# Performance work log

Hardware: AMD Instinct MI355X
Metric: run time of the kernel (lower is better)

The kernel has to match this reference:

```python
import jax, jax.numpy as jnp
import numpy as np

B, N, M, D, CD, H, DH = 2, 2048, 2048, 1024, 1024, 8, 64
INNER = H * DH  # 512
FFD = 4 * D
SCALE = DH ** -0.5


def _ln(x, g, b):
    mu = jnp.mean(x, axis=-1, keepdims=True)
    var = jnp.mean((x - mu) ** 2, axis=-1, keepdims=True)
    return (x - mu) * jax.lax.rsqrt(var + 1e-5) * g + b


def _ff(x, g, b, w1, b1, w2, b2):
    h = jax.nn.gelu(_ln(x, g, b) @ w1 + b1, approximate=False)
    return h @ w2 + b2


def setup_inputs() -> dict:
    key = jax.random.key(0)
    ks = jax.random.split(key, 16)
    s = 0.02
    return {
        'x': jax.random.normal(ks[0], (B, N, D), jnp.float32),
        'context': jax.random.normal(ks[1], (B, M, CD), jnp.float32),
        'mask': jnp.ones((B, N), bool),
        'context_mask': jnp.ones((B, M), bool),
        'ln_x_g': jnp.ones(D), 'ln_x_b': jnp.zeros(D),
        'ln_c_g': jnp.ones(CD), 'ln_c_b': jnp.zeros(CD),
        'W_qk': jax.random.normal(ks[2], (D, INNER)) * s,
        'W_v': jax.random.normal(ks[3], (D, INNER)) * s,
        'Wc_qk': jax.random.normal(ks[4], (CD, INNER)) * s,
        'Wc_v': jax.random.normal(ks[5], (CD, INNER)) * s,
        'W_out': jax.random.normal(ks[6], (INNER, D)) * s, 'b_out': jnp.zeros(D),
        'Wc_out': jax.random.normal(ks[7], (INNER, CD)) * s, 'bc_out': jnp.zeros(CD),
        'ff_g': jnp.ones(D), 'ff_b': jnp.zeros(D),
        'ff_w1': jax.random.normal(ks[8], (D, FFD)) * s, 'ff_b1': jnp.zeros(FFD),
        'ff_w2': jax.random.normal(ks[9], (FFD, D)) * s, 'ff_b2': jnp.zeros(D),
        'cff_g': jnp.ones(CD), 'cff_b': jnp.zeros(CD),
        'cff_w1': jax.random.normal(ks[10], (CD, FFD)) * s, 'cff_b1': jnp.zeros(FFD),
        'cff_w2': jax.random.normal(ks[11], (FFD, CD)) * s, 'cff_b2': jnp.zeros(CD),
    }


def reference(x, context, mask, context_mask,
              ln_x_g, ln_x_b, ln_c_g, ln_c_b,
              W_qk, W_v, Wc_qk, Wc_v, W_out, b_out, Wc_out, bc_out,
              ff_g, ff_b, ff_w1, ff_b1, ff_w2, ff_b2,
              cff_g, cff_b, cff_w1, cff_b1, cff_w2, cff_b2):
    # pre-norm bidirectional cross attention
    xn = _ln(x, ln_x_g, ln_x_b)
    cn = _ln(context, ln_c_g, ln_c_b)
    qk = (xn @ W_qk).reshape(B, N, H, DH)      # b i h d
    v = (xn @ W_v).reshape(B, N, H, DH)
    cqk = (cn @ Wc_qk).reshape(B, M, H, DH)    # b j h d
    cv = (cn @ Wc_v).reshape(B, M, H, DH)
    sim = jnp.einsum('bihd,bjhd->bhij', qk, cqk) * SCALE
    pair_mask = mask[:, None, :, None] & context_mask[:, None, None, :]
    big_neg = jnp.finfo(sim.dtype).max
    sim = jnp.where(pair_mask, sim, -big_neg)
    attn = jax.nn.softmax(sim, axis=-1)        # x attends over context (j)
    cattn = jax.nn.softmax(sim, axis=-2)       # context attends over x (i)
    out = jnp.einsum('bhij,bjhd->bihd', attn, cv).reshape(B, N, INNER)
    cout = jnp.einsum('bhij,bihd->bjhd', cattn, v).reshape(B, M, INNER)
    x = x + (out @ W_out + b_out)
    context = context + (cout @ Wc_out + bc_out)
    # dual pre-norm FFN residual
    x = _ff(x, ff_g, ff_b, ff_w1, ff_b1, ff_w2, ff_b2) + x
    context = _ff(context, cff_g, cff_b, cff_w1, cff_b1, cff_w2, cff_b2) + context
    return (x, context)
```

## Files before the change

### kernel.cpp

```cpp
#include <hip/hip_runtime.h>
#include <hip/hip_bf16.h>
#include <cmath>

typedef __hip_bfloat16 bf16;
typedef __attribute__((ext_vector_type(8))) short short8;
typedef __attribute__((ext_vector_type(4))) short short4g;
typedef __attribute__((ext_vector_type(4))) float f32x4;

#define B_     2
#define N_     2048
#define M_     2048
#define D_     1024
#define H_     8
#define DH_    64
#define INNER_ 512
#define FFD_   4096
#define ROWS   4096

__device__ __forceinline__ float b2f(bf16 x){ return __bfloat162float(x); }
__device__ __forceinline__ bf16  f2b(float x){ return __float2bfloat16(x); }
__device__ __forceinline__ float s2f(short s){
    unsigned u = ((unsigned)(unsigned short)s) << 16;
    float f; __builtin_memcpy(&f, &u, 4); return f;
}
__device__ __forceinline__ short f2s(float f){
    bf16 b = __float2bfloat16(f);
    short s; __builtin_memcpy(&s, &b, 2); return s;
}
__device__ __forceinline__ float ldx(const void* p, size_t i, bool isb){
    return isb ? __bfloat162float(((const bf16*)p)[i]) : ((const float*)p)[i];
}
__device__ __forceinline__ void stx(void* p, size_t i, float v, bool isb){
    if (isb) ((bf16*)p)[i] = f2b(v); else ((float*)p)[i] = v;
}
__device__ __forceinline__ void gld16(const bf16* g, bf16* l){
    __builtin_amdgcn_global_load_lds(
        (const __attribute__((address_space(1))) void*)g,
        (__attribute__((address_space(3))) void*)l, 16, 0, 0);
}
__device__ __forceinline__ short8 ds_read128(const bf16* p){
    unsigned a = (unsigned)(size_t)(const __attribute__((address_space(3))) bf16*)p;
    short8 r;
    asm volatile("ds_read_b128 %0, %1" : "=v"(r) : "v"(a));
    return r;
}

__global__ void probe_kernel(const void* ones, int* flag){
    unsigned w = *(const unsigned*)ones;
    *flag = (w == 0x3F803F80u) ? 1 : 0;
}

template<bool IN_EXT>
__global__ __launch_bounds__(256) void ln_kernel(const void* __restrict__ x,
    const void* __restrict__ g, const void* __restrict__ b,
    bf16* __restrict__ out, const int* __restrict__ flagp)
{
    const int C = 1024;
    bool f = (*flagp != 0);
    bool bx = IN_EXT ? f : true;
    size_t base = (size_t)blockIdx.x * C;
    int t = threadIdx.x;
    float v[4]; float s = 0.f;
#pragma unroll
    for (int q = 0; q < 4; q++){ v[q] = ldx(x, base + t + q*256, bx); s += v[q]; }
    __shared__ float red[256];
    red[t] = s; __syncthreads();
    for (int o = 128; o > 0; o >>= 1){ if (t < o) red[t] += red[t+o]; __syncthreads(); }
    float mu = red[0] * (1.0f/1024.0f);
    __syncthreads();
    s = 0.f;
#pragma unroll
    for (int q = 0; q < 4; q++){ float d = v[q]-mu; s += d*d; }
    red[t] = s; __syncthreads();
    for (int o = 128; o > 0; o >>= 1){ if (t < o) red[t] += red[t+o]; __syncthreads(); }
    float rstd = rsqrtf(red[0]*(1.0f/1024.0f) + 1e-5f);
    bf16* orow = out + base;
#pragma unroll
    for (int q = 0; q < 4; q++){
        int i = t + q*256;
        orow[i] = f2b((v[q]-mu)*rstd*ldx(g,i,f) + ldx(b,i,f));
    }
}

__global__ __launch_bounds__(256) void tcast_kernel(
    const void* __restrict__ in, bf16* __restrict__ out,
    int R, int Ccols, size_t ibs, size_t obs, int force_b16,
    const int* __restrict__ flagp)
{
    bool isb = force_b16 ? true : (*flagp != 0);
    __shared__ float T[32][33];
    size_t ib = (size_t)blockIdx.z * ibs, ob = (size_t)blockIdx.z * obs;
    int r0 = blockIdx.x * 32, c0 = blockIdx.y * 32;
    int tx = threadIdx.x & 31, ty = threadIdx.x >> 5;
#pragma unroll
    for (int rr = 0; rr < 32; rr += 8)
        T[ty + rr][tx] = ldx(in, ib + (size_t)(r0 + ty + rr) * Ccols + c0 + tx, isb);
    __syncthreads();
#pragma unroll
    for (int rr = 0; rr < 32; rr += 8)
        out[ob + (size_t)(c0 + ty + rr) * R + r0 + tx] = f2b(T[tx][ty + rr]);
}

template<int MODE, int EPI, int DP>
__global__ __launch_bounds__(256) void mfma_gemm(
    const bf16* __restrict__ A, const bf16* __restrict__ A2,
    const bf16* __restrict__ Bt,
    const void* __restrict__ bias, const void* __restrict__ bias2,
    const void* __restrict__ res,  const void* __restrict__ res2,
    void* __restrict__ C, void* __restrict__ C2,
    int K, int lda, int ldb, int ldc,
    size_t coff, size_t cstr, size_t roff, float scale, int bh0,
    int azdiv, size_t astr, size_t bstr, int zsplit,
    const int* __restrict__ flagp)
{
    __shared__ __align__(16) bf16 As[DP][128*32];
    __shared__ __align__(16) bf16 Bs[DP][128*32];
    const int t = threadIdx.x;
    const int wave = t >> 6, lane = t & 63;
    const int quad = lane >> 4, l16 = lane & 15;
    const int z = blockIdx.z;

    const bf16* Ab; const bf16* Bb;
    const void* biasp = bias; const void* resp = res; void* Cp = C;
    size_t cbase;
    if (MODE == 1){
        int bh = bh0 + z, b = bh >> 3, h = bh & 7;
        Ab = A + (size_t)b * N_ * lda + h * DH_ + (size_t)blockIdx.y * 128 * lda;
        Bb = Bt + (size_t)b * M_ * ldb + h * DH_ + (size_t)blockIdx.x * 128 * ldb;
        cbase = coff + (size_t)z * N_ * M_;
    } else {
        const bf16* Ause = A;
        if (z >= zsplit){
            if (A2)    Ause  = A2;
            if (bias2) biasp = bias2;
            if (res2)  resp  = res2;
            if (C2)    Cp    = C2;
        }
        Ab = Ause + (size_t)(z / azdiv) * astr + (size_t)blockIdx.y * 128 * lda;
        Bb = Bt + (size_t)z * bstr + (size_t)blockIdx.x * 128 * ldb;
        cbase = coff + (size_t)z * cstr;
    }

    const int c1 = t, c2 = t + 256;
    const int r1 = c1 >> 2, q1 = ((c1 & 3) - (r1 >> 1)) & 3;
    const int r2 = c2 >> 2, q2 = ((c2 & 3) - (r2 >> 1)) & 3;
    const bf16* ga1 = Ab + (size_t)r1 * lda + q1 * 8;
    const bf16* ga2 = Ab + (size_t)r2 * lda + q2 * 8;
    const bf16* gb1 = Bb + (size_t)r1 * ldb + q1 * 8;
    const bf16* gb2 = Bb + (size_t)r2 * ldb + q2 * 8;
    const int la1 = (wave * 64) * 8;
    const int la2 = (256 + wave * 64) * 8;
    const int moff = (wave & 1) * 64, noff = (wave >> 1) * 64;

    auto stage = [&](int d, int k0){
        gld16(ga1 + k0, &As[d][la1]);
        gld16(ga2 + k0, &As[d][la2]);
        gld16(gb1 + k0, &Bs[d][la1]);
        gld16(gb2 + k0, &Bs[d][la2]);
    };

    f32x4 acc[4][4];
#pragma unroll
    for (int mi = 0; mi < 4; mi++)
#pragma unroll
        for (int ni = 0; ni < 4; ni++)
#pragma unroll
            for (int r = 0; r < 4; r++) acc[mi][ni][r] = 0.f;

    const int nt = K >> 5;
    for (int d = 0; d < DP - 1; ++d)
        if (d < nt) stage(d, d * 32);

    for (int tt = 0; tt < nt; ++tt){
        if (tt + DP - 1 < nt) stage((tt + DP - 1) % DP, (tt + DP - 1) * 32);
        int rem = nt - 1 - tt;
        int lv  = rem < DP - 1 ? rem : DP - 1;
        if      (lv >= 3) asm volatile("s_waitcnt vmcnt(12)" ::: "memory");
        else if (lv == 2) asm volatile("s_waitcnt vmcnt(8)"  ::: "memory");
        else if (lv == 1) asm volatile("s_waitcnt vmcnt(4)"  ::: "memory");
        else              asm volatile("s_waitcnt vmcnt(0)"  ::: "memory");
        __builtin_amdgcn_s_barrier();
        const bf16* Al = As[tt % DP];
        const bf16* Bl = Bs[tt % DP];
        short8 af[4], bf8[4];
#pragma unroll
        for (int mi = 0; mi < 4; mi++){
            int rr = moff + mi*16 + l16;
            int qp = (quad + (rr >> 1)) & 3;
            af[mi] = ds_read128(Al + ((size_t)rr*4 + qp)*8);
        }
#pragma unroll
        for (int ni = 0; ni < 4; ni++){
            int rr = noff + ni*16 + l16;
            int qp = (quad + (rr >> 1)) & 3;
            bf8[ni] = ds_read128(Bl + ((size_t)rr*4 + qp)*8);
        }
        asm volatile("s_waitcnt lgkmcnt(0)" ::: "memory");
        __builtin_amdgcn_sched_barrier(0);
        __builtin_amdgcn_s_setprio(1);
#pragma unroll
        for (int mi = 0; mi < 4; mi++)
#pragma unroll
            for (int ni = 0; ni < 4; ni++)
                acc[mi][ni] = __builtin_amdgcn_mfma_f32_16x16x32_bf16(
                    af[mi], bf8[ni], acc[mi][ni], 0, 0, 0);
        __builtin_amdgcn_s_setprio(0);
        __builtin_amdgcn_s_barrier();
    }

    bool f = false;
    if (EPI >= 1) f = (*flagp != 0);
    const int mb = blockIdx.y * 128, nb = blockIdx.x * 128;
#pragma unroll
    for (int ni = 0; ni < 4; ni++){
        int n = nb + noff + ni*16 + l16;
        float bv = (EPI >= 1) ? ldx(biasp, n, f) : 0.0f;
#pragma unroll
        for (int mi = 0; mi < 4; mi++){
#pragma unroll
            for (int r = 0; r < 4; r++){
                int m = mb + moff + mi*16 + quad*4 + r;
                float val = acc[mi][ni][r] * scale + bv;
                if (EPI == 2) val = 0.5f*val*(1.0f + erff(val*0.70710678118f));
                size_t idx = (size_t)m * ldc + n;
                if (EPI == 3) val += ldx(resp, roff + idx, f);
                if (EPI == 4) val += b2f(((const bf16*)resp)[roff + idx]);
                if (EPI == 4) stx(Cp, cbase + idx, val, f);
                else ((bf16*)Cp)[cbase + idx] = f2b(val);
            }
        }
    }
}

#define KSTR 72
#define PSTR 136
__global__ __launch_bounds__(256) void flash_attn(
    const bf16* __restrict__ qk, const bf16* __restrict__ cqk,
    const bf16* __restrict__ vT, const bf16* __restrict__ cvT,
    bf16* __restrict__ aout, bf16* __restrict__ acout)
{
    __shared__ __align__(16) bf16 QP[64*PSTR];
    __shared__ __align__(16) bf16 Ks[128*KSTR];
    __shared__ __align__(16) bf16 Vs[64*PSTR];
    const int t = threadIdx.x;
    const int wave = t >> 6, lane = t & 63, quad = lane >> 4, l16 = lane & 15;
    const int z = blockIdx.y;
    const int dir = z >> 4, bh = z & 15, b = bh >> 3, h = bh & 7;
    const bf16 *Qg, *Kg, *Vg; bf16* Og;
    if (dir == 0){ Qg = qk;  Kg = cqk; Vg = cvT; Og = aout;  }
    else         { Qg = cqk; Kg = qk;  Vg = vT;  Og = acout; }
    const int i0 = blockIdx.x * 64;
    const bf16* Qb = Qg + ((size_t)b*2048 + i0)*INNER_ + h*DH_;
    const bf16* Kb = Kg + (size_t)b*2048*INNER_ + h*DH_;
    const bf16* Vb = Vg + ((size_t)b*INNER_ + h*DH_)*2048;

    for (int c = t; c < 64*8; c += 256){
        int r = c >> 3, jc = c & 7;
        short8 raw = *(const short8*)(Qb + (size_t)r*INNER_ + jc*8);
        short8 s;
#pragma unroll
        for (int q = 0; q < 8; q++) s[q] = f2s(s2f(raw[q]) * 0.125f);
        *(short8*)(QP + r*PSTR + jc*8) = s;
    }
    __syncthreads();
    const int moff = wave * 16;
    short8 qf[2];
#pragma unroll
    for (int ks = 0; ks < 2; ks++)
        qf[ks] = *(const short8*)(QP + (moff + l16)*PSTR + ks*32 + quad*8);

    f32x4 O[4];
    float mrow = -1e30f, lrow = 0.f;
#pragma unroll
    for (int nd = 0; nd < 4; nd++)
#pragma unroll
        for (int r = 0; r < 4; r++) O[nd][r] = 0.f;

    short8 kreg[4], vreg[4];
#pragma unroll
    for (int i = 0; i < 4; i++){
        int c = t + i*256;
        kreg[i] = *(const short8*)(Kb + (size_t)(c >> 3)*INNER_ + (c & 7)*8);
        vreg[i] = *(const short8*)(Vb + (size_t)(c >> 4)*2048 + (c & 15)*8);
    }

    for (int j0 = 0; j0 < 2048; j0 += 128){
        __syncthreads();
#pragma unroll
        for (int i = 0; i < 4; i++){
            int c = t + i*256;
            *(short8*)(Ks + (c >> 3)*KSTR + (c & 7)*8) = kreg[i];
            *(short8*)(Vs + (c >> 4)*PSTR + (c & 15)*8) = vreg[i];
        }
        __syncthreads();
        if (j0 + 128 < 2048){
#pragma unroll
            for (int i = 0; i < 4; i++){
                int c = t + i*256;
                kreg[i] = *(const short8*)(Kb + (size_t)(j0+128 + (c >> 3))*INNER_ + (c & 7)*8);
                vreg[i] = *(const short8*)(Vb + (size_t)(c >> 4)*2048 + j0+128 + (c & 15)*8);
            }
        }
        f32x4 S[8];
#pragma unroll
        for (int ni = 0; ni < 8; ni++)
#pragma unroll
            for (int r = 0; r < 4; r++) S[ni][r] = 0.f;
        __builtin_amdgcn_s_setprio(1);
#pragma unroll
        for (int ks = 0; ks < 2; ks++){
#pragma unroll
            for (int ni = 0; ni < 8; ni++){
                short8 kf = *(const short8*)(Ks + (ni*16 + l16)*KSTR + ks*32 + quad*8);
                S[ni] = __builtin_amdgcn_mfma_f32_16x16x32_bf16(
                    kf, qf[ks], S[ni], 0, 0, 0);
            }
        }
        __builtin_amdgcn_s_setprio(0);
        float rm = -1e30f;
#pragma unroll
        for (int ni = 0; ni < 8; ni++){
            float a = fmaxf(S[ni][0], S[ni][1]);
            float c2 = fmaxf(S[ni][2], S[ni][3]);
            rm = fmaxf(rm, fmaxf(a, c2));
        }
        rm = fmaxf(rm, __shfl_xor(rm, 16, 64));
        rm = fmaxf(rm, __shfl_xor(rm, 32, 64));
        float mn = fmaxf(mrow, rm);
        float al = __expf(mrow - mn);
        mrow = mn;
        float rs = 0.f;
#pragma unroll
        for (int ni = 0; ni < 8; ni++)
#pragma unroll
            for (int r = 0; r < 4; r++){
                float pv = __expf(S[ni][r] - mn);
                S[ni][r] = pv; rs += pv;
            }
        rs += __shfl_xor(rs, 16, 64);
        rs += __shfl_xor(rs, 32, 64);
        lrow = lrow*al + rs;
        float alq[4];
#pragma unroll
        for (int r = 0; r < 4; r++) alq[r] = __shfl(al, quad*4 + r, 64);
#pragma unroll
        for (int nd = 0; nd < 4; nd++)
#pragma unroll
            for (int r = 0; r < 4; r++) O[nd][r] *= alq[r];
#pragma unroll
        for (int ni = 0; ni < 8; ni++){
            short4g pk;
#pragma unroll
            for (int r = 0; r < 4; r++) pk[r] = f2s(S[ni][r]);
            *(short4g*)(QP + (moff + l16)*PSTR + ni*16 + quad*4) = pk;
        }
        __builtin_amdgcn_s_setprio(1);
#pragma unroll
        for (int ks2 = 0; ks2 < 4; ks2++){
            short8 pf = *(const short8*)(QP + (moff + l16)*PSTR + ks2*32 + quad*8);
            short8 vf[4];
#pragma unroll
            for (int nd = 0; nd < 4; nd++)
                vf[nd] = *(const short8*)(Vs + (nd*16 + l16)*PSTR + ks2*32 + quad*8);
#pragma unroll
            for (int nd = 0; nd < 4; nd++)
                O[nd] = __builtin_amdgcn_mfma_f32_16x16x32_bf16(
                    pf, vf[nd], O[nd], 0, 0, 0);
        }
        __builtin_amdgcn_s_setprio(0);
    }
    float linv[4];
#pragma unroll
    for (int r = 0; r < 4; r++) linv[r] = 1.0f / __shfl(lrow, quad*4 + r, 64);
#pragma unroll
    for (int r = 0; r < 4; r++){
        int row = i0 + moff + quad*4 + r;
#pragma unroll
        for (int nd = 0; nd < 4; nd++){
            int d = nd*16 + l16;
            Og[((size_t)b*2048 + row)*INNER_ + h*DH_ + d] = f2b(O[nd][r] * linv[r]);
        }
    }
}

extern "C" void kernel_launch(void* const* d_in, const int* in_sizes, int n_in,
                              void* d_out, int out_size, void* d_ws, size_t ws_size,
                              hipStream_t stream)
{
    const void* x      = d_in[0];
    const void* ctx    = d_in[1];
    const void* ln_x_g = d_in[4];
    const void* ln_x_b = d_in[5];
    const void* ln_c_g = d_in[6];
    const void* ln_c_b = d_in[7];
    const void* W_qk   = d_in[8];
    const void* W_v    = d_in[9];
    const void* Wc_qk  = d_in[10];
    const void* Wc_v   = d_in[11];
    const void* W_out  = d_in[12];
    const void* b_out  = d_in[13];
    const void* Wc_out = d_in[14];
    const void* bc_out = d_in[15];
    const void* ff_g   = d_in[16];
    const void* ff_b   = d_in[17];
    const void* ff_w1  = d_in[18];
    const void* ff_b1  = d_in[19];
    const void* ff_w2  = d_in[20];
    const void* ff_b2  = d_in[21];
    const void* cff_g  = d_in[22];
    const void* cff_b  = d_in[23];
    const void* cff_w1 = d_in[24];
    const void* cff_b1 = d_in[25];
    const void* cff_w2 = d_in[26];
    const void* cff_b2 = d_in[27];
    (void)in_sizes; (void)n_in; (void)out_size;

    const size_t MB = 1024ull*1024;
    char* p = (char*)d_ws;
    int*  flag = (int*)p;  p += 256;
    bf16* xn   = (bf16*)p; p += 8*MB;
    bf16* cn   = (bf16*)p; p += 8*MB;
    bf16* xmid = (bf16*)p; p += 8*MB;
    bf16* cmid = (bf16*)p; p += 8*MB;
    bf16* Wqk_t  = (bf16*)p; p += 1*MB;
    bf16* Wv_t   = (bf16*)p; p += 1*MB;
    bf16* Wcqk_t = (bf16*)p; p += 1*MB;
    bf16* Wcv_t  = (bf16*)p; p += 1*MB;
    bf16* Wout_t = (bf16*)p; p += 1*MB;
    bf16* Wcout_t= (bf16*)p; p += 1*MB;
    bf16* ffw1_t = (bf16*)p; p += 8*MB;
    bf16* ffw2_t = (bf16*)p; p += 8*MB;
    bf16* cffw1_t= (bf16*)p; p += 8*MB;
    bf16* cffw2_t= (bf16*)p; p += 8*MB;
    char* R = p; p += 32*MB;
    bf16* qk    = (bf16*)(R +  0*MB);
    bf16* vv    = (bf16*)(R +  4*MB);
    bf16* cqk   = (bf16*)(R +  8*MB);
    bf16* cv    = (bf16*)(R + 12*MB);
    bf16* aout  = (bf16*)(R + 16*MB);
    bf16* acout = (bf16*)(R + 20*MB);
    bf16* vT    = (bf16*)(R + 24*MB);
    bf16* cvT   = (bf16*)(R + 28*MB);
    bf16* hbuf  = (bf16*)R;
    p = (char*)(((size_t)p + 255) & ~(size_t)255);
    size_t fixed = (size_t)(p - (char*)d_ws);
    bf16* hbuf2 = (bf16*)p;
    bool batched_ffn = (ws_size >= fixed + 32*MB);

    probe_kernel<<<1, 1, 0, stream>>>(ln_x_g, flag);

    auto TC = [&](const void* in, bf16* o, int Rr, int Cc){
        tcast_kernel<<<dim3(Rr/32, Cc/32, 1), 256, 0, stream>>>(in, o, Rr, Cc, 0, 0, 0, flag);
    };
    TC(W_qk,   Wqk_t,  1024, 512);
    TC(W_v,    Wv_t,   1024, 512);
    TC(Wc_qk,  Wcqk_t, 1024, 512);
    TC(Wc_v,   Wcv_t,  1024, 512);
    TC(W_out,  Wout_t,  512, 1024);
    TC(Wc_out, Wcout_t, 512, 1024);
    TC(ff_w1,  ffw1_t, 1024, 4096);
    TC(ff_w2,  ffw2_t, 4096, 1024);
    TC(cff_w1, cffw1_t,1024, 4096);
    TC(cff_w2, cffw2_t,4096, 1024);

    ln_kernel<true><<<ROWS, 256, 0, stream>>>(x,   ln_x_g, ln_x_b, xn, flag);
    ln_kernel<true><<<ROWS, 256, 0, stream>>>(ctx, ln_c_g, ln_c_b, cn, flag);

    mfma_gemm<2,0,4><<<dim3(4,32,4), 256, 0, stream>>>(
        xn, nullptr, Wqk_t, nullptr, nullptr, nullptr, nullptr, qk, nullptr,
        1024, 1024, 1024, 512, 0, (size_t)ROWS*INNER_, 0, 1.f, 0,
        2, (size_t)(cn - xn), (size_t)(Wv_t - Wqk_t), 4, flag);

    tcast_kernel<<<dim3(64,16,2), 256, 0, stream>>>(vv, vT, 2048, 512,
        (size_t)N_*INNER_, (size_t)N_*INNER_, 1, flag);
    tcast_kernel<<<dim3(64,16,2), 256, 0, stream>>>(cv, cvT, 2048, 512,
        (size_t)M_*INNER_, (size_t)M_*INNER_, 1, flag);

    flash_attn<<<dim3(32, 32), 256, 0, stream>>>(qk, cqk, vT, cvT, aout, acout);

    mfma_gemm<2,3,4><<<dim3(8,32,2), 256, 0, stream>>>(
        aout, nullptr, Wout_t, b_out, bc_out, x, ctx, xmid, nullptr,
        512, 512, 512, 1024, 0, (size_t)ROWS*D_, 0, 1.f, 0,
        1, (size_t)(acout - aout), (size_t)(Wcout_t - Wout_t), 1, flag);

    if (batched_ffn){
        ln_kernel<false><<<ROWS, 256, 0, stream>>>(xmid, ff_g,  ff_b,  xn, flag);
        ln_kernel<false><<<ROWS, 256, 0, stream>>>(cmid, cff_g, cff_b, cn, flag);
        mfma_gemm<2,2,2><<<dim3(32,32,2), 256, 0, stream>>>(
            xn, nullptr, ffw1_t, ff_b1, cff_b1, nullptr, nullptr, hbuf, hbuf2,
            1024, 1024, 1024, 4096, 0, 0, 0, 1.f, 0,
            1, (size_t)(cn - xn), (size_t)(cffw1_t - ffw1_t), 1, flag);
        mfma_gemm<2,4,4><<<dim3(8,32,2), 256, 0, stream>>>(
            hbuf, hbuf2, ffw2_t, ff_b2, cff_b2, xmid, cmid, d_out, nullptr,
            4096, 4096, 4096, 1024, 0, (size_t)ROWS*D_, 0, 1.f, 0,
            1, 0, (size_t)(cffw2_t - ffw2_t), 1, flag);
    } else {
        ln_kernel<false><<<ROWS, 256, 0, stream>>>(xmid, ff_g, ff_b, xn, flag);
        mfma_gemm<2,2,2><<<dim3(32,32,1), 256, 0, stream>>>(
            xn, nullptr, ffw1_t, ff_b1, nullptr, nullptr, nullptr, hbuf, nullptr,
            1024, 1024, 1024, 4096, 0, 0, 0, 1.f, 0, 1, 0, 0, 1, flag);
        mfma_gemm<2,4,4><<<dim3(8,32,1), 256, 0, stream>>>(
            hbuf, nullptr, ffw2_t, ff_b2, nullptr, xmid, nullptr, d_out, nullptr,
            4096, 4096, 4096, 1024, 0, 0, 0, 1.f, 0, 1, 0, 0, 1, flag);
        ln_kernel<false><<<ROWS, 256, 0, stream>>>(cmid, cff_g, cff_b, cn, flag);
        mfma_gemm<2,2,2><<<dim3(32,32,1), 256, 0, stream>>>(
            cn, nullptr, cffw1_t, cff_b1, nullptr, nullptr, nullptr, hbuf, nullptr,
            1024, 1024, 1024, 4096, 0, 0, 0, 1.f, 0, 1, 0, 0, 1, flag);
        mfma_gemm<2,4,4><<<dim3(8,32,1), 256, 0, stream>>>(
            hbuf, nullptr, cffw2_t, cff_b2, nullptr, cmid, nullptr, d_out, nullptr,
            4096, 4096, 4096, 1024, (size_t)ROWS*D_, 0, 0, 1.f, 0, 1, 0, 0, 1, flag);
    }
}
```

Before: 616.0 us.

## Add 256x256-tile, 4-stage pipelined GEMM for the FFN up-projection

Adds a new gemm256 kernel with 512 threads, 256x256 output tiles, and a four-deep LDS buffer ring filled by async global-to-LDS loads with graded vmcnt waits. It uses a swizzled LDS layout and raises wave priority around the MFMA block. It replaces the 128x128 mfma_gemm for the FFN first layer with bias+GELU epilogue, aiming for more operand reuse per tile and better latency hiding. The cost is much larger LDS use (128KB) and more accumulator registers, which limits occupancy to one block per CU. It also yields only 512 blocks across the batched launch.

```diff
diff --git a/kernel.cpp b/kernel.cpp
--- a/kernel.cpp
+++ b/kernel.cpp
@@ -227,6 +227,118 @@
                 if (EPI == 4) val += b2f(((const bf16*)resp)[roff + idx]);
                 if (EPI == 4) stx(Cp, cbase + idx, val, f);
                 else ((bf16*)Cp)[cbase + idx] = f2b(val);
+            }
+        }
+    }
+}
+
+template<int EPI>
+__global__ __launch_bounds__(512) void gemm256(
+    const bf16* __restrict__ A, const bf16* __restrict__ Bt,
+    const void* __restrict__ bias, const void* __restrict__ bias2,
+    void* __restrict__ C, void* __restrict__ C2,
+    int K, int lda, int ldb, int ldc,
+    size_t astr, size_t bstr, int zsplit,
+    const int* __restrict__ flagp)
+{
+    constexpr int DP = 4;
+    __shared__ __align__(16) bf16 As[DP][256*32];
+    __shared__ __align__(16) bf16 Bs[DP][256*32];
+    const int t = threadIdx.x;
+    const int wave = t >> 6, lane = t & 63;
+    const int quad = lane >> 4, l16 = lane & 15;
+    const int z = blockIdx.z;
+    const void* biasp = bias; void* Cp = C;
+    if (z >= zsplit){
+        if (bias2) biasp = bias2;
+        if (C2)    Cp    = C2;
+    }
+    const bf16* Ab = A + (size_t)z * astr + (size_t)blockIdx.y * 256 * lda;
+    const bf16* Bb = Bt + (size_t)z * bstr + (size_t)blockIdx.x * 256 * ldb;
+
+    const int c1 = t, c2 = t + 512;
+    const int r1 = c1 >> 2, q1 = ((c1 & 3) - (r1 >> 1)) & 3;
+    const int r2 = c2 >> 2, q2 = ((c2 & 3) - (r2 >> 1)) & 3;
+    const bf16* ga1 = Ab + (size_t)r1 * lda + q1 * 8;
+    const bf16* ga2 = Ab + (size_t)r2 * lda + q2 * 8;
+    const bf16* gb1 = Bb + (size_t)r1 * ldb + q1 * 8;
+    const bf16* gb2 = Bb + (size_t)r2 * ldb + q2 * 8;
+    const int la1 = (wave * 64) * 8;
+    const int la2 = (512 + wave * 64) * 8;
+    const int moff = (wave >> 2) * 128;
+    const int noff = (wave & 3) * 64;
+
+    auto stage = [&](int d, int k0){
+        gld16(ga1 + k0, &As[d][la1]);
+        gld16(ga2 + k0, &As[d][la2]);
+        gld16(gb1 + k0, &Bs[d][la1]);
+        gld16(gb2 + k0, &Bs[d][la2]);
+    };
+
+    f32x4 acc[8][4];
+#pragma unroll
+    for (int mi = 0; mi < 8; mi++)
+#pragma unroll
+        for (int ni = 0; ni < 4; ni++)
+#pragma unroll
+            for (int r = 0; r < 4; r++) acc[mi][ni][r] = 0.f;
+
+    const int nt = K >> 5;
+    for (int d = 0; d < DP - 1; ++d)
+        if (d < nt) stage(d, d * 32);
+
+    for (int tt = 0; tt < nt; ++tt){
+        if (tt + DP - 1 < nt) stage((tt + DP - 1) % DP, (tt + DP - 1) * 32);
+        int rem = nt - 1 - tt;
+        int lv  = rem < DP - 1 ? rem : DP - 1;
+        if      (lv >= 3) asm volatile("s_waitcnt vmcnt(12)" ::: "memory");
+        else if (lv == 2) asm volatile("s_waitcnt vmcnt(8)"  ::: "memory");
+        else if (lv == 1) asm volatile("s_waitcnt vmcnt(4)"  ::: "memory");
+        else              asm volatile("s_waitcnt vmcnt(0)"  ::: "memory");
+        __builtin_amdgcn_s_barrier();
+        const bf16* Al = As[tt % DP];
+        const bf16* Bl = Bs[tt % DP];
+        short8 af[8], bf8[4];
+#pragma unroll
+        for (int mi = 0; mi < 8; mi++){
+            int rr = moff + mi*16 + l16;
+            int qp = (quad + (rr >> 1)) & 3;
+            af[mi] = ds_read128(Al + ((size_t)rr*4 + qp)*8);
+        }
+#pragma unroll
+        for (int ni = 0; ni < 4; ni++){
+            int rr = noff + ni*16 + l16;
+            int qp = (quad + (rr >> 1)) & 3;
+            bf8[ni] = ds_read128(Bl + ((size_t)rr*4 + qp)*8);
+        }
+        asm volatile("s_waitcnt lgkmcnt(0)" ::: "memory");
+        __builtin_amdgcn_sched_barrier(0);
+        __builtin_amdgcn_s_setprio(1);
+#pragma unroll
+        for (int mi = 0; mi < 8; mi++)
+#pragma unroll
+            for (int ni = 0; ni < 4; ni++)
+                acc[mi][ni] = __builtin_amdgcn_mfma_f32_16x16x32_bf16(
+                    af[mi], bf8[ni], acc[mi][ni], 0, 0, 0);
+        __builtin_amdgcn_s_setprio(0);
+        __builtin_amdgcn_s_barrier();
+    }
+
+    bool f = false;
+    if (EPI >= 1) f = (*flagp != 0);
+    const int mb = blockIdx.y * 256 + moff, nb = blockIdx.x * 256 + noff;
+#pragma unroll
+    for (int ni = 0; ni < 4; ni++){
+        int n = nb + ni*16 + l16;
+        float bv = (EPI >= 1) ? ldx(biasp, n, f) : 0.0f;
+#pragma unroll
+        for (int mi = 0; mi < 8; mi++){
+#pragma unroll
+            for (int r = 0; r < 4; r++){
+                int m = mb + mi*16 + quad*4 + r;
+                float val = acc[mi][ni][r] + bv;
+                if (EPI == 2) val = 0.5f*val*(1.0f + erff(val*0.70710678118f));
+                ((bf16*)Cp)[(size_t)m * ldc + n] = f2b(val);
             }
         }
     }
@@ -486,26 +598,26 @@
     if (batched_ffn){
         ln_kernel<false><<<ROWS, 256, 0, stream>>>(xmid, ff_g,  ff_b,  xn, flag);
         ln_kernel<false><<<ROWS, 256, 0, stream>>>(cmid, cff_g, cff_b, cn, flag);
-        mfma_gemm<2,2,2><<<dim3(32,32,2), 256, 0, stream>>>(
-            xn, nullptr, ffw1_t, ff_b1, cff_b1, nullptr, nullptr, hbuf, hbuf2,
-            1024, 1024, 1024, 4096, 0, 0, 0, 1.f, 0,
-            1, (size_t)(cn - xn), (size_t)(cffw1_t - ffw1_t), 1, flag);
+        gemm256<2><<<dim3(16,16,2), 512, 0, stream>>>(
+            xn, ffw1_t, ff_b1, cff_b1, hbuf, hbuf2,
+            1024, 1024, 1024, 4096,
+            (size_t)(cn - xn), (size_t)(cffw1_t - ffw1_t), 1, flag);
         mfma_gemm<2,4,4><<<dim3(8,32,2), 256, 0, stream>>>(
             hbuf, hbuf2, ffw2_t, ff_b2, cff_b2, xmid, cmid, d_out, nullptr,
             4096, 4096, 4096, 1024, 0, (size_t)ROWS*D_, 0, 1.f, 0,
             1, 0, (size_t)(cffw2_t - ffw2_t), 1, flag);
     } else {
         ln_kernel<false><<<ROWS, 256, 0, stream>>>(xmid, ff_g, ff_b, xn, flag);
-        mfma_gemm<2,2,2><<<dim3(32,32,1), 256, 0, stream>>>(
-            xn, nullptr, ffw1_t, ff_b1, nullptr, nullptr, nullptr, hbuf, nullptr,
-            1024, 1024, 1024, 4096, 0, 0, 0, 1.f, 0, 1, 0, 0, 1, flag);
+        gemm256<2><<<dim3(16,16,1), 512, 0, stream>>>(
+            xn, ffw1_t, ff_b1, nullptr, hbuf, nullptr,
+            1024, 1024, 1024, 4096, 0, 0, 1, flag);
         mfma_gemm<2,4,4><<<dim3(8,32,1), 256, 0, stream>>>(
             hbuf, nullptr, ffw2_t, ff_b2, nullptr, xmid, nullptr, d_out, nullptr,
             4096, 4096, 4096, 1024, 0, 0, 0, 1.f, 0, 1, 0, 0, 1, flag);
         ln_kernel<false><<<ROWS, 256, 0, stream>>>(cmid, cff_g, cff_b, cn, flag);
-        mfma_gemm<2,2,2><<<dim3(32,32,1), 256, 0, stream>>>(
-            cn, nullptr, cffw1_t, cff_b1, nullptr, nullptr, nullptr, hbuf, nullptr,
-            1024, 1024, 1024, 4096, 0, 0, 0, 1.f, 0, 1, 0, 0, 1, flag);
+        gemm256<2><<<dim3(16,16,1), 512, 0, stream>>>(
+            cn, cffw1_t, cff_b1, nullptr, hbuf, nullptr,
+            1024, 1024, 1024, 4096, 0, 0, 1, flag);
         mfma_gemm<2,4,4><<<dim3(8,32,1), 256, 0, stream>>>(
             hbuf, nullptr, cffw2_t, cff_b2, nullptr, cmid, nullptr, d_out, nullptr,
             4096, 4096, 4096, 1024, (size_t)ROWS*D_, 0, 0, 1.f, 0, 1, 0, 0, 1, flag);
```

New measurement: 632.9 us. 1.03x slower.
